# Performance work log

Hardware: AMD Instinct MI355X
Metric: run time of the kernel (lower is better)

The kernel has to match this reference:

```python
import jax, jax.numpy as jnp
import numpy as np

N_ENTITY = 64368
N_REL = 12
DIM = 128
NB = 8
N_ITEM = 6924
E = 1_000_000
B = 128
L = 32


def setup_inputs() -> dict:
    key = jax.random.key(0)
    ks = jax.random.split(key, 12)
    return {
        "edge_idx": jax.random.randint(ks[0], (2, E), 0, N_ENTITY),
        "edge_type": jax.random.randint(ks[1], (E,), 0, N_REL),
        "seed_ids": jax.random.randint(ks[2], (B, L), 0, N_ITEM),
        "seed_len": jax.random.randint(ks[3], (B,), 0, L + 1),
        "labels": jax.random.randint(ks[4], (B,), 0, N_ITEM),
        # RGCN basis-decomposition params (x=None => in_channels = n_entity)
        "basis": jax.random.normal(ks[5], (NB, N_ENTITY, DIM), dtype=jnp.float32) * 0.02,
        "att": jax.random.normal(ks[6], (N_REL, NB), dtype=jnp.float32) * 0.1,
        "root": jax.random.normal(ks[7], (N_ENTITY, DIM), dtype=jnp.float32) * 0.02,
        "rgcn_bias": jnp.zeros((DIM,), dtype=jnp.float32),
        # SelfAttentionLayer params
        "attn_a": jax.random.normal(ks[8], (DIM, DIM), dtype=jnp.float32) * 0.1,
        "attn_b": jax.random.normal(ks[9], (DIM, 1), dtype=jnp.float32) * 0.1,
        # output linear bias (weight is tied to item node features per F.linear(u, nodes, bias))
        "out_bias": jnp.zeros((N_ITEM,), dtype=jnp.float32),
    }


def _rgcn(edge_idx, edge_type, basis, att, root, rgcn_bias):
    src, dst = edge_idx[0], edge_idx[1]
    # composed per-relation weight acting as relation-specific node embeddings: [R, N, D]
    w = jnp.einsum('rb,bnd->rnd', att, basis)
    msg = w[edge_type, src]  # [E, D] relation-indexed gather
    aggr = jax.ops.segment_sum(msg, dst, num_segments=N_ENTITY)
    deg = jax.ops.segment_sum(jnp.ones((msg.shape[0],), msg.dtype), dst, num_segments=N_ENTITY)
    aggr = aggr / jnp.maximum(deg, 1.0)[:, None]  # mean aggregation
    return aggr + root + rgcn_bias  # update: aggr + root (x=None) + bias


def _pool(nodes, seed_ids, seed_len, attn_a, attn_b):
    h = nodes[seed_ids]  # [B, L, D] ragged gather (padded)
    e = (jnp.tanh(h @ attn_a) @ attn_b)[..., 0]  # [B, L]
    mask = jnp.arange(seed_ids.shape[1])[None, :] < seed_len[:, None]
    attn = jax.nn.softmax(jnp.where(mask, e, -1e9), axis=-1)
    u = jnp.einsum('bl,bld->bd', attn, h)
    return jnp.where((seed_len > 0)[:, None], u, 0.0)  # empty seed set -> zeros


def reference(edge_idx, edge_type, seed_ids, seed_len, labels,
              basis, att, root, rgcn_bias, attn_a, attn_b, out_bias):
    nodes = _rgcn(edge_idx, edge_type, basis, att, root, rgcn_bias)  # [N, D]
    u = _pool(nodes, seed_ids, seed_len, attn_a, attn_b)             # [B, D]
    scores = u @ nodes[:N_ITEM].T + out_bias                          # [B, N_ITEM]
    return scores
```

## Files before the change

kernel.cpp:

```cpp
#include <hip/hip_runtime.h>
#include <math.h>

#define N_ENTITY 64368
#define N_REL 12
#define DIM 128
#define NB 8
#define N_ITEM 6924
#define NEDGE 1000000
#define BATCH 128
#define SEQL 32
#define ITEM_TILE 32
#define CAP 96
#define CAP2 32

__global__ __launch_bounds__(256) void fill_kernel(
    const int* __restrict__ e_src, const int* __restrict__ e_dst,
    const int* __restrict__ e_type, int* __restrict__ cursorD,
    int* __restrict__ cursorS, int* __restrict__ bucketS)
{
    int gid = blockIdx.x * 256 + threadIdx.x;
    if (gid * 4 >= NEDGE) return;
    int4 s4 = reinterpret_cast<const int4*>(e_src)[gid];
    int4 d4 = reinterpret_cast<const int4*>(e_dst)[gid];
    int4 t4 = reinterpret_cast<const int4*>(e_type)[gid];

    #pragma unroll
    for (int k = 0; k < 4; ++k) {
        int s = (k == 0) ? s4.x : (k == 1) ? s4.y : (k == 2) ? s4.z : s4.w;
        int d = (k == 0) ? d4.x : (k == 1) ? d4.y : (k == 2) ? d4.z : d4.w;
        int t = (k == 0) ? t4.x : (k == 1) ? t4.y : (k == 2) ? t4.z : t4.w;
        if (d < N_ITEM) {
            int pos = atomicAdd(&cursorD[d], 1);
            if (pos < CAP) {
                int slot = d * CAP + pos;
                int p2 = atomicAdd(&cursorS[s], 1);
                if (p2 < CAP2) bucketS[s * CAP2 + p2] = slot | (t << 20);
            }
        }
    }
}

__global__ __launch_bounds__(256) void msg_kernel(
    const int* __restrict__ cursorS, const int* __restrict__ bucketS,
    const float* __restrict__ basis, const float* __restrict__ att,
    float* __restrict__ msg)
{
    __shared__ float att_s[N_REL * NB];
    if (threadIdx.x < N_REL * NB) att_s[threadIdx.x] = att[threadIdx.x];
    __syncthreads();

    int wave = threadIdx.x >> 6;
    int lane = threadIdx.x & 63;
    int s    = blockIdx.x * 4 + wave;
    if (s >= N_ENTITY) return;

    int n = cursorS[s];
    if (n <= 0) return;
    if (n > CAP2) n = CAP2;

    float2 v[NB];
    const float* bp = basis + (size_t)s * DIM + lane * 2;
    #pragma unroll
    for (int b = 0; b < NB; ++b)
        v[b] = *reinterpret_cast<const float2*>(bp + (size_t)b * (N_ENTITY * DIM));

    int pk = 0;
    if (lane < n) pk = bucketS[s * CAP2 + lane];

    for (int j = 0; j < n; ++j) {
        int p    = __shfl(pk, j);
        int slot = p & 0xFFFFF;
        int tt   = p >> 20;
        float mx = 0.f, my = 0.f;
        #pragma unroll
        for (int b = 0; b < NB; ++b) {
            float a = att_s[tt * NB + b];
            mx += a * v[b].x;
            my += a * v[b].y;
        }
        *reinterpret_cast<float2*>(msg + (size_t)slot * DIM + lane * 2)
            = make_float2(mx, my);
    }
}

__global__ __launch_bounds__(256) void reduce_kernel(
    const int* __restrict__ cursorD, const float* __restrict__ msg,
    const float* __restrict__ root, const float* __restrict__ bias,
    float* __restrict__ nodes)
{
    int wave = threadIdx.x >> 6;
    int lane = threadIdx.x & 63;
    int half = lane >> 5;
    int l32  = lane & 31;
    int row  = blockIdx.x * 4 + wave;
    if (row >= N_ITEM) return;

    int deg = cursorD[row];
    int n   = (deg > CAP) ? CAP : deg;

    float4 acc = make_float4(0.f, 0.f, 0.f, 0.f);
    const float* mp = msg + (size_t)row * CAP * DIM + (l32 << 2);
    for (int i = half; i < n; i += 2) {
        float4 m = *reinterpret_cast<const float4*>(mp + (size_t)i * DIM);
        acc.x += m.x; acc.y += m.y; acc.z += m.z; acc.w += m.w;
    }
    acc.x += __shfl_xor(acc.x, 32);
    acc.y += __shfl_xor(acc.y, 32);
    acc.z += __shfl_xor(acc.z, 32);
    acc.w += __shfl_xor(acc.w, 32);

    if (half == 0) {
        float  inv = 1.0f / fmaxf((float)deg, 1.0f);
        float4 r   = *reinterpret_cast<const float4*>(root + (size_t)row * DIM + (l32 << 2));
        float4 bs  = *reinterpret_cast<const float4*>(bias + (l32 << 2));
        float4 o;
        o.x = acc.x * inv + r.x + bs.x;
        o.y = acc.y * inv + r.y + bs.y;
        o.z = acc.z * inv + r.z + bs.z;
        o.w = acc.w * inv + r.w + bs.w;
        *reinterpret_cast<float4*>(nodes + (size_t)row * DIM + (l32 << 2)) = o;
    }
}

__global__ __launch_bounds__(256) void pool_kernel(
    const float* __restrict__ nodes, const int* __restrict__ seed_ids,
    const int* __restrict__ seed_len, const float* __restrict__ attn_a,
    const float* __restrict__ attn_b, float* __restrict__ u)
{
    __shared__ float h[SEQL * 132];
    __shared__ float ev[SEQL];
    __shared__ float attw[SEQL];
    __shared__ int   seeds[SEQL];

    int b   = blockIdx.x;
    int tid = threadIdx.x;
    int len = seed_len[b];

    if (tid < SEQL) seeds[tid] = seed_ids[b * SEQL + tid];
    __syncthreads();

    for (int idx = tid; idx < SEQL * (DIM / 4); idx += 256) {
        int l  = idx >> 5;
        int kq = idx & 31;
        float4 v = reinterpret_cast<const float4*>(nodes)[(size_t)seeds[l] * 32 + kq];
        *reinterpret_cast<float4*>(h + l * 132 + kq * 4) = v;
    }
    __syncthreads();

    {
        int l = tid >> 3;
        int j = tid & 7;
        float dot[16];
        #pragma unroll
        for (int i = 0; i < 16; ++i) dot[i] = 0.f;
        const float* hr = h + l * 132;
        for (int k = 0; k < DIM; ++k) {
            float hv = hr[k];
            const float4* ar = reinterpret_cast<const float4*>(attn_a + k * DIM + j * 16);
            float4 a0 = ar[0], a1 = ar[1], a2 = ar[2], a3 = ar[3];
            dot[0]  += hv * a0.x; dot[1]  += hv * a0.y; dot[2]  += hv * a0.z; dot[3]  += hv * a0.w;
            dot[4]  += hv * a1.x; dot[5]  += hv * a1.y; dot[6]  += hv * a1.z; dot[7]  += hv * a1.w;
            dot[8]  += hv * a2.x; dot[9]  += hv * a2.y; dot[10] += hv * a2.z; dot[11] += hv * a2.w;
            dot[12] += hv * a3.x; dot[13] += hv * a3.y; dot[14] += hv * a3.z; dot[15] += hv * a3.w;
        }
        float sum = 0.f;
        #pragma unroll
        for (int i = 0; i < 16; ++i) sum += tanhf(dot[i]) * attn_b[j * 16 + i];
        sum += __shfl_xor(sum, 1);
        sum += __shfl_xor(sum, 2);
        sum += __shfl_xor(sum, 4);
        if (j == 0) ev[l] = sum;
    }
    __syncthreads();

    if (tid < SEQL) {
        float val = (tid < len) ? ev[tid] : -3.0e38f;
        float m = val;
        #pragma unroll
        for (int off = 16; off > 0; off >>= 1) m = fmaxf(m, __shfl_xor(m, off));
        float p = (tid < len) ? expf(val - m) : 0.f;
        float ssum = p;
        #pragma unroll
        for (int off = 16; off > 0; off >>= 1) ssum += __shfl_xor(ssum, off);
        attw[tid] = (len > 0) ? p / ssum : 0.f;
    }
    __syncthreads();

    if (tid < DIM) {
        float acc = 0.f;
        #pragma unroll
        for (int l = 0; l < SEQL; ++l) acc += attw[l] * h[l * 132 + tid];
        u[(size_t)b * DIM + tid] = acc;
    }
}

__global__ __launch_bounds__(256) void score_kernel(
    const float* __restrict__ nodes, const float* __restrict__ u,
    const float* __restrict__ out_bias, float* __restrict__ out)
{
    __shared__ float us[BATCH * DIM];
    __shared__ float ns[ITEM_TILE * 132];
    int tid   = threadIdx.x;
    int item0 = blockIdx.x * ITEM_TILE;

    for (int idx = tid; idx < BATCH * (DIM / 4); idx += 256)
        reinterpret_cast<float4*>(us)[idx] = reinterpret_cast<const float4*>(u)[idx];

    for (int idx = tid; idx < ITEM_TILE * (DIM / 4); idx += 256) {
        int j  = idx >> 5;
        int kq = idx & 31;
        int item = item0 + j;
        float4 v = make_float4(0.f, 0.f, 0.f, 0.f);
        if (item < N_ITEM) v = reinterpret_cast<const float4*>(nodes)[(size_t)item * 32 + kq];
        *reinterpret_cast<float4*>(ns + j * 132 + kq * 4) = v;
    }
    __syncthreads();

    int jg = tid & 15;
    int bg = tid >> 4;
    float acc0[8], acc1[8];
    #pragma unroll
    for (int i = 0; i < 8; ++i) { acc0[i] = 0.f; acc1[i] = 0.f; }
    const float* n0p = ns + (jg * 2 + 0) * 132;
    const float* n1p = ns + (jg * 2 + 1) * 132;
    for (int k = 0; k < DIM; k += 4) {
        float4 n0 = *reinterpret_cast<const float4*>(n0p + k);
        float4 n1 = *reinterpret_cast<const float4*>(n1p + k);
        #pragma unroll
        for (int bb = 0; bb < 8; ++bb) {
            float4 uv = *reinterpret_cast<const float4*>(us + (bg * 8 + bb) * DIM + k);
            acc0[bb] += uv.x * n0.x + uv.y * n0.y + uv.z * n0.z + uv.w * n0.w;
            acc1[bb] += uv.x * n1.x + uv.y * n1.y + uv.z * n1.z + uv.w * n1.w;
        }
    }
    #pragma unroll
    for (int bb = 0; bb < 8; ++bb) {
        int bi  = bg * 8 + bb;
        int it0 = item0 + jg * 2;
        if (it0     < N_ITEM) out[(size_t)bi * N_ITEM + it0]     = acc0[bb] + out_bias[it0];
        if (it0 + 1 < N_ITEM) out[(size_t)bi * N_ITEM + it0 + 1] = acc1[bb] + out_bias[it0 + 1];
    }
}

extern "C" void kernel_launch(void* const* d_in, const int* in_sizes, int n_in,
                              void* d_out, int out_size, void* d_ws, size_t ws_size,
                              hipStream_t stream)
{
    const int*   e_src     = (const int*)d_in[0];
    const int*   e_dst     = e_src + NEDGE;
    const int*   e_type    = (const int*)d_in[1];
    const int*   seed_ids  = (const int*)d_in[2];
    const int*   seed_len  = (const int*)d_in[3];
    const float* basis     = (const float*)d_in[5];
    const float* att       = (const float*)d_in[6];
    const float* root      = (const float*)d_in[7];
    const float* rgcn_bias = (const float*)d_in[8];
    const float* attn_a    = (const float*)d_in[9];
    const float* attn_b    = (const float*)d_in[10];
    const float* out_bias  = (const float*)d_in[11];
    float*       out       = (float*)d_out;

    int*   cursorD = (int*)d_ws;
    int*   cursorS = cursorD + 6928;
    int*   bucketS = cursorS + 64384;
    float* msg     = (float*)(bucketS + (size_t)N_ENTITY * CAP2);
    float* nodes   = msg + (size_t)N_ITEM * CAP * DIM;
    float* u       = nodes + (size_t)N_ITEM * DIM;

    hipMemsetAsync(cursorD, 0, (6928 + 64384) * sizeof(int), stream);

    fill_kernel<<<(NEDGE / 4 + 255) / 256, 256, 0, stream>>>(
        e_src, e_dst, e_type, cursorD, cursorS, bucketS);
    msg_kernel<<<(N_ENTITY + 3) / 4, 256, 0, stream>>>(
        cursorS, bucketS, basis, att, msg);
    reduce_kernel<<<(N_ITEM + 3) / 4, 256, 0, stream>>>(
        cursorD, msg, rgcn_bias ? root : root, rgcn_bias, nodes);
    pool_kernel<<<BATCH, 256, 0, stream>>>(
        nodes, seed_ids, seed_len, attn_a, attn_b, u);
    score_kernel<<<(N_ITEM + ITEM_TILE - 1) / ITEM_TILE, 256, 0, stream>>>(
        nodes, u, out_bias, out);
}
```

Baseline: 487.5 us.

## Replace per-edge message buffer with direct float atomics into destination accumulators

Removes the CAP-slotted per-destination message buffer and its separate reduction pass. Each source-entity half-wave now computes its relation-composed message and atomically adds it straight into a compact [N_ITEM, DIM] accumulator, followed by a flat elementwise finalize that applies the mean, root and bias. This avoids writing and re-reading about 340MB of message storage, at the cost of contended float atomics and a larger memset. Summation order becomes nondeterministic, and the old per-destination CAP truncation of in-degree is dropped.

```diff
diff --git a/kernel.cpp b/kernel.cpp
--- a/kernel.cpp
+++ b/kernel.cpp
@@ -10,7 +10,6 @@
 #define BATCH 128
 #define SEQL 32
 #define ITEM_TILE 32
-#define CAP 96
 #define CAP2 32
 
 __global__ __launch_bounds__(256) void fill_kernel(
@@ -30,96 +29,82 @@
         int d = (k == 0) ? d4.x : (k == 1) ? d4.y : (k == 2) ? d4.z : d4.w;
         int t = (k == 0) ? t4.x : (k == 1) ? t4.y : (k == 2) ? t4.z : t4.w;
         if (d < N_ITEM) {
-            int pos = atomicAdd(&cursorD[d], 1);
-            if (pos < CAP) {
-                int slot = d * CAP + pos;
-                int p2 = atomicAdd(&cursorS[s], 1);
-                if (p2 < CAP2) bucketS[s * CAP2 + p2] = slot | (t << 20);
-            }
-        }
-    }
-}
-
-__global__ __launch_bounds__(256) void msg_kernel(
+            atomicAdd(&cursorD[d], 1);
+            int p2 = atomicAdd(&cursorS[s], 1);
+            if (p2 < CAP2) bucketS[s * CAP2 + p2] = d | (t << 13);
+        }
+    }
+}
+
+__global__ __launch_bounds__(256) void accum_kernel(
     const int* __restrict__ cursorS, const int* __restrict__ bucketS,
     const float* __restrict__ basis, const float* __restrict__ att,
-    float* __restrict__ msg)
+    float* __restrict__ acc)
 {
     __shared__ float att_s[N_REL * NB];
     if (threadIdx.x < N_REL * NB) att_s[threadIdx.x] = att[threadIdx.x];
     __syncthreads();
 
-    int wave = threadIdx.x >> 6;
-    int lane = threadIdx.x & 63;
-    int s    = blockIdx.x * 4 + wave;
-    if (s >= N_ENTITY) return;
-
-    int n = cursorS[s];
-    if (n <= 0) return;
-    if (n > CAP2) n = CAP2;
-
-    float2 v[NB];
-    const float* bp = basis + (size_t)s * DIM + lane * 2;
-    #pragma unroll
-    for (int b = 0; b < NB; ++b)
-        v[b] = *reinterpret_cast<const float2*>(bp + (size_t)b * (N_ENTITY * DIM));
-
-    int pk = 0;
-    if (lane < n) pk = bucketS[s * CAP2 + lane];
-
-    for (int j = 0; j < n; ++j) {
-        int p    = __shfl(pk, j);
-        int slot = p & 0xFFFFF;
-        int tt   = p >> 20;
-        float mx = 0.f, my = 0.f;
-        #pragma unroll
-        for (int b = 0; b < NB; ++b) {
-            float a = att_s[tt * NB + b];
-            mx += a * v[b].x;
-            my += a * v[b].y;
-        }
-        *reinterpret_cast<float2*>(msg + (size_t)slot * DIM + lane * 2)
-            = make_float2(mx, my);
-    }
-}
-
-__global__ __launch_bounds__(256) void reduce_kernel(
-    const int* __restrict__ cursorD, const float* __restrict__ msg,
-    const float* __restrict__ root, const float* __restrict__ bias,
-    float* __restrict__ nodes)
-{
     int wave = threadIdx.x >> 6;
     int lane = threadIdx.x & 63;
     int half = lane >> 5;
     int l32  = lane & 31;
-    int row  = blockIdx.x * 4 + wave;
-    if (row >= N_ITEM) return;
-
-    int deg = cursorD[row];
-    int n   = (deg > CAP) ? CAP : deg;
-
-    float4 acc = make_float4(0.f, 0.f, 0.f, 0.f);
-    const float* mp = msg + (size_t)row * CAP * DIM + (l32 << 2);
-    for (int i = half; i < n; i += 2) {
-        float4 m = *reinterpret_cast<const float4*>(mp + (size_t)i * DIM);
-        acc.x += m.x; acc.y += m.y; acc.z += m.z; acc.w += m.w;
-    }
-    acc.x += __shfl_xor(acc.x, 32);
-    acc.y += __shfl_xor(acc.y, 32);
-    acc.z += __shfl_xor(acc.z, 32);
-    acc.w += __shfl_xor(acc.w, 32);
-
-    if (half == 0) {
-        float  inv = 1.0f / fmaxf((float)deg, 1.0f);
-        float4 r   = *reinterpret_cast<const float4*>(root + (size_t)row * DIM + (l32 << 2));
-        float4 bs  = *reinterpret_cast<const float4*>(bias + (l32 << 2));
-        float4 o;
-        o.x = acc.x * inv + r.x + bs.x;
-        o.y = acc.y * inv + r.y + bs.y;
-        o.z = acc.z * inv + r.z + bs.z;
-        o.w = acc.w * inv + r.w + bs.w;
-        *reinterpret_cast<float4*>(nodes + (size_t)row * DIM + (l32 << 2)) = o;
-    }
+    int s    = blockIdx.x * 8 + wave * 2 + half;
+    if (s >= N_ENTITY) return;
+
+    int n = cursorS[s];
+    if (n <= 0) return;
+    if (n > CAP2) n = CAP2;
+
+    float4 v[NB];
+    const float* bp = basis + (size_t)s * DIM + (l32 << 2);
+    #pragma unroll
+    for (int b = 0; b < NB; ++b)
+        v[b] = *reinterpret_cast<const float4*>(bp + (size_t)b * (N_ENTITY * DIM));
+
+    int pk = 0;
+    if (l32 < n) pk = bucketS[s * CAP2 + l32];
+
+    for (int j = 0; j < n; ++j) {
+        int p = __shfl(pk, (half << 5) + j);
+        int d = p & 0x1FFF;
+        int t = p >> 13;
+        float4 m = make_float4(0.f, 0.f, 0.f, 0.f);
+        #pragma unroll
+        for (int b = 0; b < NB; ++b) {
+            float a = att_s[t * NB + b];
+            m.x += a * v[b].x;
+            m.y += a * v[b].y;
+            m.z += a * v[b].z;
+            m.w += a * v[b].w;
+        }
+        float* dst = acc + (size_t)d * DIM + (l32 << 2);
+        unsafeAtomicAdd(dst + 0, m.x);
+        unsafeAtomicAdd(dst + 1, m.y);
+        unsafeAtomicAdd(dst + 2, m.z);
+        unsafeAtomicAdd(dst + 3, m.w);
+    }
+}
+
+__global__ __launch_bounds__(256) void finalize_kernel(
+    const int* __restrict__ cursorD, const float* __restrict__ acc,
+    const float* __restrict__ root, const float* __restrict__ bias,
+    float* __restrict__ nodes)
+{
+    int gid = blockIdx.x * 256 + threadIdx.x;
+    if (gid >= N_ITEM * (DIM / 4)) return;
+    int row = gid >> 5;
+    int q   = gid & 31;
+    float inv = 1.0f / fmaxf((float)cursorD[row], 1.0f);
+    float4 a = reinterpret_cast<const float4*>(acc)[gid];
+    float4 r = reinterpret_cast<const float4*>(root)[gid];
+    float4 b = reinterpret_cast<const float4*>(bias)[q];
+    float4 o;
+    o.x = a.x * inv + r.x + b.x;
+    o.y = a.y * inv + r.y + b.y;
+    o.z = a.z * inv + r.z + b.z;
+    o.w = a.w * inv + r.w + b.w;
+    reinterpret_cast<float4*>(nodes)[gid] = o;
 }
 
 __global__ __launch_bounds__(256) void pool_kernel(
@@ -262,19 +247,20 @@
 
     int*   cursorD = (int*)d_ws;
     int*   cursorS = cursorD + 6928;
-    int*   bucketS = cursorS + 64384;
-    float* msg     = (float*)(bucketS + (size_t)N_ENTITY * CAP2);
-    float* nodes   = msg + (size_t)N_ITEM * CAP * DIM;
+    float* acc     = (float*)(cursorS + 64384);
+    int*   bucketS = (int*)(acc + (size_t)N_ITEM * DIM);
+    float* nodes   = (float*)(bucketS + (size_t)N_ENTITY * CAP2);
     float* u       = nodes + (size_t)N_ITEM * DIM;
 
-    hipMemsetAsync(cursorD, 0, (6928 + 64384) * sizeof(int), stream);
+    hipMemsetAsync(cursorD, 0,
+                   (6928 + 64384 + (size_t)N_ITEM * DIM) * sizeof(int), stream);
 
     fill_kernel<<<(NEDGE / 4 + 255) / 256, 256, 0, stream>>>(
         e_src, e_dst, e_type, cursorD, cursorS, bucketS);
-    msg_kernel<<<(N_ENTITY + 3) / 4, 256, 0, stream>>>(
-        cursorS, bucketS, basis, att, msg);
-    reduce_kernel<<<(N_ITEM + 3) / 4, 256, 0, stream>>>(
-        cursorD, msg, rgcn_bias ? root : root, rgcn_bias, nodes);
+    accum_kernel<<<(N_ENTITY + 7) / 8, 256, 0, stream>>>(
+        cursorS, bucketS, basis, att, acc);
+    finalize_kernel<<<(N_ITEM * (DIM / 4) + 255) / 256, 256, 0, stream>>>(
+        cursorD, acc, root, rgcn_bias, nodes);
     pool_kernel<<<BATCH, 256, 0, stream>>>(
         nodes, seed_ids, seed_len, attn_a, attn_b, u);
     score_kernel<<<(N_ITEM + ITEM_TILE - 1) / ITEM_TILE, 256, 0, stream>>>(
```

After: 568.0 us. 1.17x slower.
